# Kernel tuning notes

Hardware: AMD Instinct MI355X
Metric: run time of the kernel (lower is better)

## Reference

```python
import jax, jax.numpy as jnp
import numpy as np

B, T, L, F = 32, 512, 16, 128   # utterances, max frames, frame-spec width, specgram_height
H = 128                          # hidden_size1 == hidden_size2
C = 61                           # TIMIT phoneme count


def _p(key, shape, scale):
    return jax.random.normal(key, shape, jnp.float32) * scale


def setup_inputs() -> dict:
    key = jax.random.key(0)
    ks = jax.random.split(key, 32)
    s = 1.0 / np.sqrt(H)
    inp = {}
    inp["x"] = jax.random.normal(ks[0], (B, T, L, F), jnp.float32)
    inp["lengths"] = jax.random.randint(ks[1], (B,), T // 2, T + 1, jnp.int32)
    i = 2
    # rnn1: tanh-RNN, 2 layers, bidirectional (layer0 in=F, layer1 in=2H); dir axis 0
    for name, din in (("r1l0", F), ("r1l1", 2 * H)):
        inp[name + "_Wih"] = _p(ks[i], (2, H, din), s); i += 1
        inp[name + "_Whh"] = _p(ks[i], (2, H, H), s); i += 1
        inp[name + "_bih"] = _p(ks[i], (2, H), s); i += 1
        inp[name + "_bhh"] = _p(ks[i], (2, H), s); i += 1
    # rnn2: GRU, 2 layers, bidirectional (in=2H for both layers); gates packed r,z,n
    for name in ("g0", "g1"):
        inp[name + "_Wih"] = _p(ks[i], (2, 3 * H, 2 * H), s); i += 1
        inp[name + "_Whh"] = _p(ks[i], (2, 3 * H, H), s); i += 1
        inp[name + "_bih"] = _p(ks[i], (2, 3 * H), s); i += 1
        inp[name + "_bhh"] = _p(ks[i], (2, 3 * H), s); i += 1
    inp["fc_W"] = _p(ks[i], (C, 2 * H), s); i += 1
    inp["fc_b"] = _p(ks[i], (C,), s)
    return inp


def _rnn_bidir(x, Wih, Whh, bih, bhh):
    # x: (N, S, din) -> (N, S, 2H); PyTorch nn.RNN(tanh), bidirectional
    outs = []
    for d in range(2):
        xw = jnp.einsum('bli,hi->blh', x, Wih[d]) + bih[d]
        W, b = Whh[d], bhh[d]
        def step(h, xt):
            h = jnp.tanh(xt + h @ W.T + b)
            return h, h
        h0 = jnp.zeros((x.shape[0], W.shape[0]), x.dtype)
        _, ys = jax.lax.scan(step, h0, jnp.swapaxes(xw, 0, 1), reverse=(d == 1))
        outs.append(jnp.swapaxes(ys, 0, 1))
    return jnp.concatenate(outs, -1)


def _gru_bidir(x, Wih, Whh, bih, bhh):
    # x: (N, S, din) -> (N, S, 2H); PyTorch nn.GRU, bidirectional
    outs = []
    for d in range(2):
        xw = jnp.einsum('bli,hi->blh', x, Wih[d]) + bih[d]  # (N, S, 3H)
        W, b = Whh[d], bhh[d]
        def step(h, xt):
            g = h @ W.T + b
            xr, xz, xn = jnp.split(xt, 3, -1)
            gr, gz, gn = jnp.split(g, 3, -1)
            r = jax.nn.sigmoid(xr + gr)
            z = jax.nn.sigmoid(xz + gz)
            n = jnp.tanh(xn + r * gn)
            h = (1.0 - z) * n + z * h
            return h, h
        h0 = jnp.zeros((x.shape[0], W.shape[1]), x.dtype)
        _, ys = jax.lax.scan(step, h0, jnp.swapaxes(xw, 0, 1), reverse=(d == 1))
        outs.append(jnp.swapaxes(ys, 0, 1))
    return jnp.concatenate(outs, -1)


def reference(x, lengths,
              r1l0_Wih, r1l0_Whh, r1l0_bih, r1l0_bhh,
              r1l1_Wih, r1l1_Whh, r1l1_bih, r1l1_bhh,
              g0_Wih, g0_Whh, g0_bih, g0_bhh,
              g1_Wih, g1_Whh, g1_bih, g1_bhh,
              fc_W, fc_b):
    b, t, l, f = x.shape
    # per-sample rnn1 loop == one batched pass over all B*T frames (eval mode: no dropout)
    o = _rnn_bidir(x.reshape(b * t, l, f), r1l0_Wih, r1l0_Whh, r1l0_bih, r1l0_bhh)
    o = _rnn_bidir(o, r1l1_Wih, r1l1_Whh, r1l1_bih, r1l1_bhh)
    o = o[:, -1, :].reshape(b, t, 2 * H)       # last inner timestep per frame
    o = _gru_bidir(o, g0_Wih, g0_Whh, g0_bih, g0_bhh)
    o = _gru_bidir(o, g1_Wih, g1_Whh, g1_bih, g1_bhh)
    logits = o @ fc_W.T + fc_b                  # (B, T, C)
    mask = jnp.arange(t)[None, :] < lengths[:, None]
    # ragged scatter: concat first lengths[i] timesteps of each sample
    return logits.reshape(b * t, -1)[mask.reshape(-1)]
```

## Files before the change

kernel.cpp:

```cpp
#include <hip/hip_runtime.h>
#include <hip/hip_bf16.h>

#define B_ 32
#define T_ 512
#define L_ 16
#define F_ 128
#define H_ 128
#define C_ 61
#define NF_ (B_*T_)
#define CH_ 4096

typedef unsigned int u32;
typedef unsigned short u16;
typedef __attribute__((ext_vector_type(8))) short s16x8;
typedef __attribute__((ext_vector_type(4))) float f32x4;

__device__ __forceinline__ float bflo(u32 v){ return __uint_as_float(v << 16); }
__device__ __forceinline__ float bfhi(u32 v){ return __uint_as_float(v & 0xffff0000u); }
__device__ __forceinline__ u16 f2bf(float f){
  u32 u = __float_as_uint(f);
  u += 0x7fffu + ((u >> 16) & 1u);
  return (u16)(u >> 16);
}
__device__ __forceinline__ u32 pack2(float a, float b){
  return (u32)f2bf(a) | ((u32)f2bf(b) << 16);
}
__device__ __forceinline__ float fast_tanh(float x){
  float e = __expf(2.f*x);
  return 1.f - 2.f*__builtin_amdgcn_rcpf(e + 1.f);
}
__device__ __forceinline__ float fast_sigmoid(float x){
  return __builtin_amdgcn_rcpf(1.f + __expf(-x));
}
__device__ __forceinline__ f32x4 mfma16(s16x8 a, s16x8 b, f32x4 c){
  return __builtin_amdgcn_mfma_f32_16x16x32_bf16(a, b, c, 0, 0, 0);
}
__device__ __forceinline__ s16x8 packfrag(const float* p){
  const float4 a = *(const float4*)p;
  const float4 b = *(const float4*)(p+4);
  union { s16x8 v; u32 w[4]; } f;
  f.w[0]=pack2(a.x,a.y); f.w[1]=pack2(a.z,a.w);
  f.w[2]=pack2(b.x,b.y); f.w[3]=pack2(b.z,b.w);
  return f.v;
}

__global__ __launch_bounds__(256) void l0_mfma(
    const float* __restrict__ x,
    const float* __restrict__ Wih,
    const float* __restrict__ Whh,
    const float* __restrict__ bih,
    const float* __restrict__ bhh,
    u16* __restrict__ out)
{
  __shared__ __align__(16) u16 Hb[2][32][136];
  __shared__ __align__(16) u16 Xb[2][32][136];
  const int t = threadIdx.x;
  const int lane = t & 63, wv = t >> 6;
  const int l15 = lane & 15, kg = lane >> 4;
  const int dir = blockIdx.y;
  const int f0 = blockIdx.x * 32;
  s16x8 wih[2][4], whh[2][4];
  {
    const float* Wid = Wih + dir*16384;
    const float* Whd = Whh + dir*16384;
    #pragma unroll
    for (int nt = 0; nt < 2; nt++){
      const int u = wv*32 + nt*16 + l15;
      #pragma unroll
      for (int kc = 0; kc < 4; kc++){
        const int k = kc*32 + kg*8;
        wih[nt][kc] = packfrag(&Wid[u*128 + k]);
        whh[nt][kc] = packfrag(&Whd[u*128 + k]);
      }
    }
  }
  float bv[2];
  bv[0] = bih[dir*128 + wv*32 + l15]      + bhh[dir*128 + wv*32 + l15];
  bv[1] = bih[dir*128 + wv*32 + 16 + l15] + bhh[dir*128 + wv*32 + 16 + l15];
  const int sr = t >> 3, sc = (t & 7) * 16;
  {
    *(uint4*)&Hb[0][sr][sc]   = make_uint4(0,0,0,0);
    *(uint4*)&Hb[0][sr][sc+8] = make_uint4(0,0,0,0);
    const int s0 = dir ? 15 : 0;
    const float4* xp = (const float4*)&x[(size_t)(f0+sr)*2048 + s0*128 + sc];
    const float4 v0 = xp[0], v1 = xp[1], v2 = xp[2], v3 = xp[3];
    *(uint4*)&Xb[0][sr][sc]   = make_uint4(pack2(v0.x,v0.y),pack2(v0.z,v0.w),
                                           pack2(v1.x,v1.y),pack2(v1.z,v1.w));
    *(uint4*)&Xb[0][sr][sc+8] = make_uint4(pack2(v2.x,v2.y),pack2(v2.z,v2.w),
                                           pack2(v3.x,v3.y),pack2(v3.z,v3.w));
  }
  __syncthreads();
  int cur = 0;
  for (int st = 0; st < 16; st++){
    const int s = dir ? (15-st) : st;
    float4 p0,p1,p2,p3;
    if (st < 15){
      const int sn = dir ? (14-st) : (st+1);
      const float4* xp = (const float4*)&x[(size_t)(f0+sr)*2048 + sn*128 + sc];
      p0 = xp[0]; p1 = xp[1]; p2 = xp[2]; p3 = xp[3];
    }
    f32x4 acc00 = {0.f,0.f,0.f,0.f}, acc01 = acc00, acc10 = acc00, acc11 = acc00;
    #pragma unroll
    for (int kc = 0; kc < 4; kc++){
      const int ko = kc*32 + kg*8;
      const s16x8 ax0 = *(const s16x8*)&Xb[cur][l15][ko];
      const s16x8 ax1 = *(const s16x8*)&Xb[cur][16+l15][ko];
      const s16x8 ah0 = *(const s16x8*)&Hb[cur][l15][ko];
      const s16x8 ah1 = *(const s16x8*)&Hb[cur][16+l15][ko];
      acc00 = mfma16(ax0, wih[0][kc], acc00);
      acc01 = mfma16(ax0, wih[1][kc], acc01);
      acc10 = mfma16(ax1, wih[0][kc], acc10);
      acc11 = mfma16(ax1, wih[1][kc], acc11);
      acc00 = mfma16(ah0, whh[0][kc], acc00);
      acc01 = mfma16(ah0, whh[1][kc], acc01);
      acc10 = mfma16(ah1, whh[0][kc], acc10);
      acc11 = mfma16(ah1, whh[1][kc], acc11);
    }
    const int u0 = wv*32 + l15, u1 = wv*32 + 16 + l15;
    u16* op = out + (size_t)f0*4096 + s*256 + dir*128;
    #pragma unroll
    for (int r = 0; r < 4; r++){
      const int m0r = kg*4 + r, m1r = 16 + kg*4 + r;
      u16 h00 = f2bf(fast_tanh(acc00[r] + bv[0]));
      u16 h01 = f2bf(fast_tanh(acc01[r] + bv[1]));
      u16 h10 = f2bf(fast_tanh(acc10[r] + bv[0]));
      u16 h11 = f2bf(fast_tanh(acc11[r] + bv[1]));
      Hb[cur^1][m0r][u0] = h00;
      Hb[cur^1][m0r][u1] = h01;
      Hb[cur^1][m1r][u0] = h10;
      Hb[cur^1][m1r][u1] = h11;
      op[(size_t)m0r*4096 + u0] = h00;
      op[(size_t)m0r*4096 + u1] = h01;
      op[(size_t)m1r*4096 + u0] = h10;
      op[(size_t)m1r*4096 + u1] = h11;
    }
    if (st < 15){
      *(uint4*)&Xb[cur^1][sr][sc]   = make_uint4(pack2(p0.x,p0.y),pack2(p0.z,p0.w),
                                                 pack2(p1.x,p1.y),pack2(p1.z,p1.w));
      *(uint4*)&Xb[cur^1][sr][sc+8] = make_uint4(pack2(p2.x,p2.y),pack2(p2.z,p2.w),
                                                 pack2(p3.x,p3.y),pack2(p3.z,p3.w));
    }
    __syncthreads();
    cur ^= 1;
  }
}

__global__ __launch_bounds__(256) void l1f_mfma(
    const u16* __restrict__ U,
    const float* __restrict__ Wih,
    const float* __restrict__ Whh,
    const float* __restrict__ bih,
    const float* __restrict__ bhh,
    u16* __restrict__ out)
{
  __shared__ __align__(16) u16 Hb[2][16][136];
  __shared__ __align__(16) u16 Xb[2][16][264];
  const int t = threadIdx.x;
  const int lane = t & 63, wv = t >> 6;
  const int l15 = lane & 15, kg = lane >> 4;
  const int f0 = blockIdx.x * 16;
  s16x8 wih[2][8], whh[2][4];
  {
    #pragma unroll
    for (int nt = 0; nt < 2; nt++){
      const int u = wv*32 + nt*16 + l15;
      #pragma unroll
      for (int kc = 0; kc < 8; kc++)
        wih[nt][kc] = packfrag(&Wih[u*256 + kc*32 + kg*8]);
      #pragma unroll
      for (int kc = 0; kc < 4; kc++)
        whh[nt][kc] = packfrag(&Whh[u*128 + kc*32 + kg*8]);
    }
  }
  float bv[2];
  bv[0] = bih[wv*32 + l15]      + bhh[wv*32 + l15];
  bv[1] = bih[wv*32 + 16 + l15] + bhh[wv*32 + 16 + l15];
  const int sr = t >> 4, scu = (t & 15) * 16;
  for (int idx = t; idx < 272; idx += 256)
    ((uint4*)&Hb[0][0][0])[idx] = make_uint4(0,0,0,0);
  {
    const uint4* up = (const uint4*)&U[(size_t)(f0+sr)*4096 + scu];
    uint4 c0 = up[0], c1 = up[1];
    *(uint4*)&Xb[0][sr][scu]   = c0;
    *(uint4*)&Xb[0][sr][scu+8] = c1;
  }
  __syncthreads();
  int cur = 0;
  for (int st = 0; st < 16; st++){
    uint4 c0,c1;
    if (st < 15){
      const uint4* up = (const uint4*)&U[(size_t)(f0+sr)*4096 + (st+1)*256 + scu];
      c0 = up[0]; c1 = up[1];
    }
    f32x4 acc0 = {0.f,0.f,0.f,0.f}, acc1 = acc0;
    #pragma unroll
    for (int kc = 0; kc < 8; kc++){
      const s16x8 ax = *(const s16x8*)&Xb[cur][l15][kc*32 + kg*8];
      acc0 = mfma16(ax, wih[0][kc], acc0);
      acc1 = mfma16(ax, wih[1][kc], acc1);
    }
    #pragma unroll
    for (int kc = 0; kc < 4; kc++){
      const s16x8 ah = *(const s16x8*)&Hb[cur][l15][kc*32 + kg*8];
      acc0 = mfma16(ah, whh[0][kc], acc0);
      acc1 = mfma16(ah, whh[1][kc], acc1);
    }
    const int u0 = wv*32 + l15, u1 = wv*32 + 16 + l15;
    #pragma unroll
    for (int r = 0; r < 4; r++){
      const int m = kg*4 + r;
      const u16 h0 = f2bf(fast_tanh(acc0[r] + bv[0]));
      const u16 h1 = f2bf(fast_tanh(acc1[r] + bv[1]));
      Hb[cur^1][m][u0] = h0;
      Hb[cur^1][m][u1] = h1;
      if (st == 15){
        out[(size_t)(f0+m)*256 + u0] = h0;
        out[(size_t)(f0+m)*256 + u1] = h1;
      }
    }
    if (st < 15){
      *(uint4*)&Xb[cur^1][sr][scu]   = c0;
      *(uint4*)&Xb[cur^1][sr][scu+8] = c1;
    }
    __syncthreads();
    cur ^= 1;
  }
}

__global__ __launch_bounds__(256) void mfma_gemm(
    const u16* __restrict__ A, int lda,
    const u16* __restrict__ Wb, int K,
    const float* __restrict__ bias,
    float* __restrict__ Cf, u16* __restrict__ Cb, int ldc, int act)
{
  const int t = threadIdx.x;
  const int lane = t & 63, wv = t >> 6;
  const int l15 = lane & 15, kg = lane >> 4;
  const int n0 = blockIdx.x * 32;
  const int m0 = blockIdx.y * 64 + wv*16;
  const u16* Ap = A + (size_t)(m0 + l15)*lda + kg*8;
  const u16* W0 = Wb + (size_t)(n0 + l15)*K + kg*8;
  const u16* W1 = Wb + (size_t)(n0 + 16 + l15)*K + kg*8;
  f32x4 acc0 = {0.f,0.f,0.f,0.f}, acc1 = acc0;
  #pragma unroll 4
  for (int kc = 0; kc < K/32; kc++){
    const s16x8 a  = *(const s16x8*)(Ap + kc*32);
    const s16x8 b0 = *(const s16x8*)(W0 + kc*32);
    const s16x8 b1 = *(const s16x8*)(W1 + kc*32);
    acc0 = mfma16(a, b0, acc0);
    acc1 = mfma16(a, b1, acc1);
  }
  const int col0 = n0 + l15, col1 = n0 + 16 + l15;
  const float bv0 = bias[col0], bv1 = bias[col1];
  #pragma unroll
  for (int r = 0; r < 4; r++){
    const int row = m0 + kg*4 + r;
    float v0 = acc0[r] + bv0, v1 = acc1[r] + bv1;
    if (act){ v0 = fast_tanh(v0); v1 = fast_tanh(v1); }
    if (Cf){
      Cf[(size_t)row*ldc + col0] = v0;
      Cf[(size_t)row*ldc + col1] = v1;
    } else {
      Cb[(size_t)row*ldc + col0] = f2bf(v0);
      Cb[(size_t)row*ldc + col1] = f2bf(v1);
    }
  }
}

__global__ __launch_bounds__(256) void gemm_xw(
    const u16* __restrict__ A, int lda,
    const u16* __restrict__ Wb, int K,
    const float* __restrict__ bih, const float* __restrict__ bhhp,
    float* __restrict__ xwT)
{
  const int t = threadIdx.x;
  const int lane = t & 63, wv = t >> 6;
  const int l15 = lane & 15, kg = lane >> 4;
  const int n0 = blockIdx.x * 32;
  const int m0 = blockIdx.y * 64 + wv*16;
  const u16* Ap = A + (size_t)(m0 + l15)*lda + kg*8;
  const u16* W0 = Wb + (size_t)(n0 + l15)*K + kg*8;
  const u16* W1 = Wb + (size_t)(n0 + 16 + l15)*K + kg*8;
  f32x4 acc0 = {0.f,0.f,0.f,0.f}, acc1 = acc0;
  #pragma unroll 4
  for (int kc = 0; kc < K/32; kc++){
    const s16x8 a  = *(const s16x8*)(Ap + kc*32);
    const s16x8 b0 = *(const s16x8*)(W0 + kc*32);
    const s16x8 b1 = *(const s16x8*)(W1 + kc*32);
    acc0 = mfma16(a, b0, acc0);
    acc1 = mfma16(a, b1, acc1);
  }
  const int col0 = n0 + l15, col1 = n0 + 16 + l15;
  const int row0 = m0 + kg*4;
  const int b = row0 >> 9, tt0 = row0 & 511;
  const int half = b >> 4, bl = b & 15;
  float bv0 = bih[col0], bv1 = bih[col1];
  {
    const int c0 = col0 >= 384 ? col0-384 : col0;
    const int c1 = col1 >= 384 ? col1-384 : col1;
    if ((c0 >> 7) < 2) bv0 += bhhp[col0];
    if ((c1 >> 7) < 2) bv1 += bhhp[col1];
  }
  size_t i0, i1;
  {
    const int d0 = col0 >= 384 ? 1 : 0;
    const int c  = col0 - d0*384;
    const int g = c >> 7, cu = c & 127;
    i0 = (((((size_t)d0*512 + tt0)*2 + half)*4 + (cu>>5))*4 + ((cu>>2)&3))*384
         + (size_t)bl*24 + ((cu>>4)&1)*12 + g*4 + (cu&3);
  }
  {
    const int d1 = col1 >= 384 ? 1 : 0;
    const int c  = col1 - d1*384;
    const int g = c >> 7, cu = c & 127;
    i1 = (((((size_t)d1*512 + tt0)*2 + half)*4 + (cu>>5))*4 + ((cu>>2)&3))*384
         + (size_t)bl*24 + ((cu>>4)&1)*12 + g*4 + (cu&3);
  }
  #pragma unroll
  for (int r = 0; r < 4; r++){
    xwT[i0 + (size_t)r*12288] = acc0[r] + bv0;
    xwT[i1 + (size_t)r*12288] = acc1[r] + bv1;
  }
}

__global__ __launch_bounds__(256) void prep_kernel(
    const float* __restrict__ g0W, const float* __restrict__ g1W,
    const float* __restrict__ r1Wih,
    const float* __restrict__ r1bih, const float* __restrict__ r1bhh,
    u16* __restrict__ g0o, u16* __restrict__ g1o, u16* __restrict__ r1o,
    float* __restrict__ bo)
{
  const int i = blockIdx.x*256 + threadIdx.x;
  if (i < 196608){ g0o[i] = f2bf(g0W[i]); g1o[i] = f2bf(g1W[i]); }
  if (i < 32768)   r1o[i] = f2bf(r1Wih[32768 + i]);
  if (i < 128)     bo[i]  = r1bih[128+i] + r1bhh[128+i];
}

__global__ __launch_bounds__(256, 1) void gru_mfma(
    const float* __restrict__ xwT,
    const float* __restrict__ Whh,
    const float* __restrict__ bhh,
    u16* __restrict__ hout)
{
  __shared__ __align__(16) u16 h_lds[2][16][136];
  const int t = threadIdx.x;
  const int lane = t & 63, wv = t >> 6;
  const int l15 = lane & 15, kg = lane >> 4;
  const int dir = blockIdx.x & 1, half = blockIdx.x >> 1;
  s16x8 wa[2][3][4];
  {
    const float* Wd = Whh + (size_t)dir*49152;
    #pragma unroll
    for (int t2 = 0; t2 < 2; t2++)
      #pragma unroll
      for (int g = 0; g < 3; g++)
        #pragma unroll
        for (int kc = 0; kc < 4; kc++)
          wa[t2][g][kc] = packfrag(&Wd[(size_t)(g*128 + wv*32 + t2*16 + l15)*128
                                       + kc*32 + kg*8]);
  }
  f32x4 bhn[2];
  bhn[0] = *(const f32x4*)&bhh[dir*384 + 256 + wv*32 + kg*4];
  bhn[1] = *(const f32x4*)&bhh[dir*384 + 256 + wv*32 + 16 + kg*4];
  {
    const uint4 z = make_uint4(0,0,0,0);
    ((uint4*)h_lds)[t] = z;
    if (t < 16) ((uint4*)h_lds)[256 + t] = z;
  }
  f32x4 hreg[2] = {{0.f,0.f,0.f,0.f},{0.f,0.f,0.f,0.f}};
  const long tstep = dir ? -49152L : 49152L;
  const char* xb = (const char*)xwT
      + ((size_t)dir*512 + (dir ? 511 : 0))*49152
      + (size_t)((((half*4 + wv)*4 + kg)*16 + l15)*24)*4;
  f32x4 pa[6], pb[6];
  #pragma unroll
  for (int j = 0; j < 6; j++) pa[j] = *(const f32x4*)(xb + j*16);
  xb += tstep;
  #pragma unroll
  for (int j = 0; j < 6; j++) pb[j] = *(const f32x4*)(xb + j*16);
  xb += tstep;
  const int hstep = dir ? -256 : 256;
  int hoff = ((half*16 + l15)*512 + (dir ? 511 : 0))*256 + dir*128 + wv*32 + kg*4;
  __syncthreads();
  int cur = 0;

#define GSTEP(PX, DOLOAD)                                                   \
  {                                                                         \
    f32x4 acc[2][3] = {{{0.f,0.f,0.f,0.f},{0.f,0.f,0.f,0.f},               \
                        {0.f,0.f,0.f,0.f}},                                 \
                       {{0.f,0.f,0.f,0.f},{0.f,0.f,0.f,0.f},               \
                        {0.f,0.f,0.f,0.f}}};                                \
    _Pragma("unroll")                                                       \
    for (int kc = 0; kc < 4; kc++){                                         \
      const s16x8 hf = *(const s16x8*)&h_lds[cur][l15][kc*32 + kg*8];       \
      _Pragma("unroll")                                                     \
      for (int t2 = 0; t2 < 2; t2++)                                        \
        _Pragma("unroll")                                                   \
        for (int g = 0; g < 3; g++)                                         \
          acc[t2][g] = mfma16(wa[t2][g][kc], hf, acc[t2][g]);               \
    }                                                                       \
    f32x4 nx0,nx1,nx2,nx3,nx4,nx5;                                          \
    if (DOLOAD){                                                            \
      nx0 = *(const f32x4*)(xb);     nx1 = *(const f32x4*)(xb+16);          \
      nx2 = *(const f32x4*)(xb+32);  nx3 = *(const f32x4*)(xb+48);          \
      nx4 = *(const f32x4*)(xb+64);  nx5 = *(const f32x4*)(xb+80);          \
      xb += tstep;                                                          \
    }                                                                       \
    _Pragma("unroll")                                                       \
    for (int t2 = 0; t2 < 2; t2++){                                         \
      float hn[4];                                                          \
      _Pragma("unroll")                                                     \
      for (int r = 0; r < 4; r++){                                          \
        const float rr = fast_sigmoid(PX[t2*3+0][r] + acc[t2][0][r]);       \
        const float zz = fast_sigmoid(PX[t2*3+1][r] + acc[t2][1][r]);       \
        const float nn = fast_tanh(PX[t2*3+2][r]                            \
                                   + rr*(acc[t2][2][r] + bhn[t2][r]));      \
        hn[r] = fmaf(zz, hreg[t2][r] - nn, nn);                             \
        hreg[t2][r] = hn[r];                                                \
      }                                                                     \
      const uint2 hp = make_uint2(pack2(hn[0],hn[1]), pack2(hn[2],hn[3]));  \
      *(uint2*)&h_lds[cur^1][l15][wv*32 + t2*16 + kg*4] = hp;               \
      *(uint2*)&hout[hoff + t2*16] = hp;                                    \
    }                                                                       \
    hoff += hstep;                                                          \
    if (DOLOAD){                                                            \
      PX[0]=nx0; PX[1]=nx1; PX[2]=nx2; PX[3]=nx3; PX[4]=nx4; PX[5]=nx5;     \
    }                                                                       \
    __syncthreads();                                                        \
    cur ^= 1;                                                               \
  }

  for (int ti = 0; ti < 510; ti += 2){
    GSTEP(pa, 1);
    GSTEP(pb, 1);
  }
  GSTEP(pa, 0);
  GSTEP(pb, 0);
#undef GSTEP
}

__global__ void prefix_kernel(const int* __restrict__ lengths, int* __restrict__ pre){
  if (threadIdx.x == 0 && blockIdx.x == 0){
    int run = 0;
    for (int b = 0; b < 32; b++){ pre[b] = run; run += lengths[b]; }
  }
}

__global__ __launch_bounds__(256) void fc_kernel(
    const u16* __restrict__ A,
    const float* __restrict__ W,
    const float* __restrict__ bias,
    const int* __restrict__ lengths,
    const int* __restrict__ pre,
    float* __restrict__ out)
{
  __shared__ __align__(16) float4 Wl[64][61];
  __shared__ __align__(16) float  Al[64][256];
  const int t = threadIdx.x;
  const int row0 = blockIdx.x * 64;
  for (int idx = t; idx < 61*64; idx += 256){
    int c = idx >> 6, k4 = idx & 63;
    Wl[k4][c] = *(const float4*)&W[(size_t)c*256 + k4*4];
  }
  {
    const u32* A32 = (const u32*)(A + (size_t)row0*256);
    for (int idx = t; idx < 8192; idx += 256){
      u32 v = A32[idx];
      int r = idx >> 7, kp = idx & 127;
      Al[r][2*kp]   = bflo(v);
      Al[r][2*kp+1] = bfhi(v);
    }
  }
  __syncthreads();
  const int c = t & 63;
  const int rbase = t >> 6;
  if (c < 61){
    const float bv = bias[c];
    for (int rr = rbase; rr < 64; rr += 4){
      float s0=0,s1=0,s2=0,s3=0;
      const float4* Ap = (const float4*)&Al[rr][0];
      #pragma unroll
      for (int k4 = 0; k4 < 64; k4++){
        const float4 w = Wl[k4][c];
        const float4 a = Ap[k4];
        s0 = fmaf(w.x, a.x, s0);
        s1 = fmaf(w.y, a.y, s1);
        s2 = fmaf(w.z, a.z, s2);
        s3 = fmaf(w.w, a.w, s3);
      }
      const int n = row0 + rr;
      const int b = n >> 9, tt = n & 511;
      if (tt < lengths[b])
        out[(size_t)(pre[b] + tt)*61 + c] = bv + s0+s1+s2+s3;
    }
  }
}

extern "C" void kernel_launch(void* const* d_in, const int* in_sizes, int n_in,
                              void* d_out, int out_size, void* d_ws, size_t ws_size,
                              hipStream_t stream)
{
  const float* x     = (const float*)d_in[0];
  const int*   lens  = (const int*)d_in[1];
  const float* r0Wih = (const float*)d_in[2];
  const float* r0Whh = (const float*)d_in[3];
  const float* r0bih = (const float*)d_in[4];
  const float* r0bhh = (const float*)d_in[5];
  const float* r1Wih = (const float*)d_in[6];
  const float* r1Whh = (const float*)d_in[7];
  const float* r1bih = (const float*)d_in[8];
  const float* r1bhh = (const float*)d_in[9];
  const float* g0Wih = (const float*)d_in[10];
  const float* g0Whh = (const float*)d_in[11];
  const float* g0bih = (const float*)d_in[12];
  const float* g0bhh = (const float*)d_in[13];
  const float* g1Wih = (const float*)d_in[14];
  const float* g1Whh = (const float*)d_in[15];
  const float* g1bih = (const float*)d_in[16];
  const float* g1bhh = (const float*)d_in[17];
  const float* fcW   = (const float*)d_in[18];
  const float* fcb   = (const float*)d_in[19];
  float* out = (float*)d_out;

  char* ws = (char*)d_ws;
  u16*   l0buf = (u16*)(ws);
  float* xwbuf = (float*)(ws);
  u16*   g0out = (u16*)(ws + 50331648);
  u16*   g0Wb  = (u16*)(ws + 58720256);
  u16*   g1Wb  = (u16*)(ws + 58720256 + 393216);
  u16*   r1Wb  = (u16*)(ws + 58720256 + 786432);
  float* biasb = (float*)(ws + 58720256 + 851968);
  u16*   g1out = (u16*)(ws + 58720256);
  u16*   rnn1  = (u16*)(ws + 67108864);
  int*   pre   = (int*)(ws + 75497472);

  prep_kernel<<<768, 256, 0, stream>>>(g0Wih, g1Wih, r1Wih, r1bih, r1bhh,
                                       g0Wb, g1Wb, r1Wb, biasb);
  for (int c = 0; c < NF_/CH_; c++){
    l0_mfma<<<dim3(CH_/32, 2), 256, 0, stream>>>(
        x + (size_t)c*CH_*2048, r0Wih, r0Whh, r0bih, r0bhh, l0buf);
    l1f_mfma<<<dim3(CH_/16), 256, 0, stream>>>(
        l0buf, r1Wih, r1Whh, r1bih, r1bhh, rnn1 + (size_t)c*CH_*256);
    mfma_gemm<<<dim3(128/32, CH_/64), 256, 0, stream>>>(
        l0buf + 15*256, 4096, r1Wb, 256, biasb,
        (float*)nullptr, rnn1 + (size_t)c*CH_*256 + 128, 256, 1);
  }
  gemm_xw<<<dim3(768/32, NF_/64), 256, 0, stream>>>(
      rnn1, 256, g0Wb, 256, g0bih, g0bhh, xwbuf);
  gru_mfma<<<4, 256, 0, stream>>>(xwbuf, g0Whh, g0bhh, g0out);
  gemm_xw<<<dim3(768/32, NF_/64), 256, 0, stream>>>(
      g0out, 256, g1Wb, 256, g1bih, g1bhh, xwbuf);
  gru_mfma<<<4, 256, 0, stream>>>(xwbuf, g1Whh, g1bhh, g1out);
  prefix_kernel<<<1, 64, 0, stream>>>(lens, pre);
  fc_kernel<<<NF_/64, 256, 0, stream>>>(g1out, fcW, fcb, lens, pre, out);
}
```

Baseline: 1.191 ms.

## Split GRU recurrence across 8 waves, halve l0 tile, use lgkm-only barriers

The latency-bound GRU recurrence now launches 512 threads per block, so each wave owns 16 hidden units instead of 32. This halves the serial MFMA chain and gate math per timestep, and the xw layout written by gemm_xw is rearranged to match. The layer-0 RNN kernel processes 16 frames per block instead of 32, doubling the block count to raise parallelism. __syncthreads is replaced by a barrier that waits only on LDS counters, avoiding stalls on outstanding global loads. The trade-off is more barrier participants per step in the GRU and relying on correct waitcnt semantics for the prefetched global loads.

```diff
diff --git a/kernel.cpp b/kernel.cpp
--- a/kernel.cpp
+++ b/kernel.cpp
@@ -35,6 +35,9 @@
 __device__ __forceinline__ f32x4 mfma16(s16x8 a, s16x8 b, f32x4 c){
   return __builtin_amdgcn_mfma_f32_16x16x32_bf16(a, b, c, 0, 0, 0);
 }
+__device__ __forceinline__ void lds_barrier(){
+  asm volatile("s_waitcnt lgkmcnt(0)\n\ts_barrier" ::: "memory");
+}
 __device__ __forceinline__ s16x8 packfrag(const float* p){
   const float4 a = *(const float4*)p;
   const float4 b = *(const float4*)(p+4);
@@ -52,13 +55,13 @@
     const float* __restrict__ bhh,
     u16* __restrict__ out)
 {
-  __shared__ __align__(16) u16 Hb[2][32][136];
-  __shared__ __align__(16) u16 Xb[2][32][136];
+  __shared__ __align__(16) u16 Hb[2][16][136];
+  __shared__ __align__(16) u16 Xb[2][16][136];
   const int t = threadIdx.x;
   const int lane = t & 63, wv = t >> 6;
   const int l15 = lane & 15, kg = lane >> 4;
   const int dir = blockIdx.y;
-  const int f0 = blockIdx.x * 32;
+  const int f0 = blockIdx.x * 16;
   s16x8 wih[2][4], whh[2][4];
   {
     const float* Wid = Wih + dir*16384;
@@ -77,70 +80,54 @@
   float bv[2];
   bv[0] = bih[dir*128 + wv*32 + l15]      + bhh[dir*128 + wv*32 + l15];
   bv[1] = bih[dir*128 + wv*32 + 16 + l15] + bhh[dir*128 + wv*32 + 16 + l15];
-  const int sr = t >> 3, sc = (t & 7) * 16;
-  {
-    *(uint4*)&Hb[0][sr][sc]   = make_uint4(0,0,0,0);
-    *(uint4*)&Hb[0][sr][sc+8] = make_uint4(0,0,0,0);
+  const int sr = t >> 4, sc8 = (t & 15) * 8;
+  for (int idx = t; idx < 272; idx += 256)
+    ((uint4*)&Hb[0][0][0])[idx] = make_uint4(0,0,0,0);
+  {
     const int s0 = dir ? 15 : 0;
-    const float4* xp = (const float4*)&x[(size_t)(f0+sr)*2048 + s0*128 + sc];
-    const float4 v0 = xp[0], v1 = xp[1], v2 = xp[2], v3 = xp[3];
-    *(uint4*)&Xb[0][sr][sc]   = make_uint4(pack2(v0.x,v0.y),pack2(v0.z,v0.w),
-                                           pack2(v1.x,v1.y),pack2(v1.z,v1.w));
-    *(uint4*)&Xb[0][sr][sc+8] = make_uint4(pack2(v2.x,v2.y),pack2(v2.z,v2.w),
-                                           pack2(v3.x,v3.y),pack2(v3.z,v3.w));
-  }
-  __syncthreads();
+    const float4* xp = (const float4*)&x[(size_t)(f0+sr)*2048 + s0*128 + sc8];
+    const float4 v0 = xp[0], v1 = xp[1];
+    *(uint4*)&Xb[0][sr][sc8] = make_uint4(pack2(v0.x,v0.y),pack2(v0.z,v0.w),
+                                          pack2(v1.x,v1.y),pack2(v1.z,v1.w));
+  }
+  lds_barrier();
   int cur = 0;
   for (int st = 0; st < 16; st++){
     const int s = dir ? (15-st) : st;
-    float4 p0,p1,p2,p3;
+    float4 p0,p1;
     if (st < 15){
       const int sn = dir ? (14-st) : (st+1);
-      const float4* xp = (const float4*)&x[(size_t)(f0+sr)*2048 + sn*128 + sc];
-      p0 = xp[0]; p1 = xp[1]; p2 = xp[2]; p3 = xp[3];
-    }
-    f32x4 acc00 = {0.f,0.f,0.f,0.f}, acc01 = acc00, acc10 = acc00, acc11 = acc00;
+      const float4* xp = (const float4*)&x[(size_t)(f0+sr)*2048 + sn*128 + sc8];
+      p0 = xp[0]; p1 = xp[1];
+    }
+    f32x4 acc0 = {0.f,0.f,0.f,0.f}, acc1 = acc0;
     #pragma unroll
     for (int kc = 0; kc < 4; kc++){
       const int ko = kc*32 + kg*8;
-      const s16x8 ax0 = *(const s16x8*)&Xb[cur][l15][ko];
-      const s16x8 ax1 = *(const s16x8*)&Xb[cur][16+l15][ko];
-      const s16x8 ah0 = *(const s16x8*)&Hb[cur][l15][ko];
-      const s16x8 ah1 = *(const s16x8*)&Hb[cur][16+l15][ko];
-      acc00 = mfma16(ax0, wih[0][kc], acc00);
-      acc01 = mfma16(ax0, wih[1][kc], acc01);
-      acc10 = mfma16(ax1, wih[0][kc], acc10);
-      acc11 = mfma16(ax1, wih[1][kc], acc11);
-      acc00 = mfma16(ah0, whh[0][kc], acc00);
-      acc01 = mfma16(ah0, whh[1][kc], acc01);
-      acc10 = mfma16(ah1, whh[0][kc], acc10);
-      acc11 = mfma16(ah1, whh[1][kc], acc11);
+      const s16x8 ax = *(const s16x8*)&Xb[cur][l15][ko];
+      const s16x8 ah = *(const s16x8*)&Hb[cur][l15][ko];
+      acc0 = mfma16(ax, wih[0][kc], acc0);
+      acc1 = mfma16(ax, wih[1][kc], acc1);
+      acc0 = mfma16(ah, whh[0][kc], acc0);
+      acc1 = mfma16(ah, whh[1][kc], acc1);
     }
     const int u0 = wv*32 + l15, u1 = wv*32 + 16 + l15;
     u16* op = out + (size_t)f0*4096 + s*256 + dir*128;
     #pragma unroll
     for (int r = 0; r < 4; r++){
-      const int m0r = kg*4 + r, m1r = 16 + kg*4 + r;
-      u16 h00 = f2bf(fast_tanh(acc00[r] + bv[0]));
-      u16 h01 = f2bf(fast_tanh(acc01[r] + bv[1]));
-      u16 h10 = f2bf(fast_tanh(acc10[r] + bv[0]));
-      u16 h11 = f2bf(fast_tanh(acc11[r] + bv[1]));
-      Hb[cur^1][m0r][u0] = h00;
-      Hb[cur^1][m0r][u1] = h01;
-      Hb[cur^1][m1r][u0] = h10;
-      Hb[cur^1][m1r][u1] = h11;
-      op[(size_t)m0r*4096 + u0] = h00;
-      op[(size_t)m0r*4096 + u1] = h01;
-      op[(size_t)m1r*4096 + u0] = h10;
-      op[(size_t)m1r*4096 + u1] = h11;
+      const int m = kg*4 + r;
+      const u16 h0 = f2bf(fast_tanh(acc0[r] + bv[0]));
+      const u16 h1 = f2bf(fast_tanh(acc1[r] + bv[1]));
+      Hb[cur^1][m][u0] = h0;
+      Hb[cur^1][m][u1] = h1;
+      op[(size_t)m*4096 + u0] = h0;
+      op[(size_t)m*4096 + u1] = h1;
     }
     if (st < 15){
-      *(uint4*)&Xb[cur^1][sr][sc]   = make_uint4(pack2(p0.x,p0.y),pack2(p0.z,p0.w),
-                                                 pack2(p1.x,p1.y),pack2(p1.z,p1.w));
-      *(uint4*)&Xb[cur^1][sr][sc+8] = make_uint4(pack2(p2.x,p2.y),pack2(p2.z,p2.w),
-                                                 pack2(p3.x,p3.y),pack2(p3.z,p3.w));
-    }
-    __syncthreads();
+      *(uint4*)&Xb[cur^1][sr][sc8] = make_uint4(pack2(p0.x,p0.y),pack2(p0.z,p0.w),
+                                                pack2(p1.x,p1.y),pack2(p1.z,p1.w));
+    }
+    lds_barrier();
     cur ^= 1;
   }
 }
@@ -184,7 +171,7 @@
     *(uint4*)&Xb[0][sr][scu]   = c0;
     *(uint4*)&Xb[0][sr][scu+8] = c1;
   }
-  __syncthreads();
+  lds_barrier();
   int cur = 0;
   for (int st = 0; st < 16; st++){
     uint4 c0,c1;
@@ -222,7 +209,7 @@
       *(uint4*)&Xb[cur^1][sr][scu]   = c0;
       *(uint4*)&Xb[cur^1][sr][scu+8] = c1;
     }
-    __syncthreads();
+    lds_barrier();
     cur ^= 1;
   }
 }
@@ -306,15 +293,15 @@
     const int d0 = col0 >= 384 ? 1 : 0;
     const int c  = col0 - d0*384;
     const int g = c >> 7, cu = c & 127;
-    i0 = (((((size_t)d0*512 + tt0)*2 + half)*4 + (cu>>5))*4 + ((cu>>2)&3))*384
-         + (size_t)bl*24 + ((cu>>4)&1)*12 + g*4 + (cu&3);
+    i0 = (((size_t)d0*512 + tt0)*2 + half)*6144
+         + (size_t)(((cu>>4)*4 + ((cu>>2)&3))*16 + bl)*12 + g*4 + (cu&3);
   }
   {
     const int d1 = col1 >= 384 ? 1 : 0;
     const int c  = col1 - d1*384;
     const int g = c >> 7, cu = c & 127;
-    i1 = (((((size_t)d1*512 + tt0)*2 + half)*4 + (cu>>5))*4 + ((cu>>2)&3))*384
-         + (size_t)bl*24 + ((cu>>4)&1)*12 + g*4 + (cu&3);
+    i1 = (((size_t)d1*512 + tt0)*2 + half)*6144
+         + (size_t)(((cu>>4)*4 + ((cu>>2)&3))*16 + bl)*12 + g*4 + (cu&3);
   }
   #pragma unroll
   for (int r = 0; r < 4; r++){
@@ -336,7 +323,7 @@
   if (i < 128)     bo[i]  = r1bih[128+i] + r1bhh[128+i];
 }
 
-__global__ __launch_bounds__(256, 1) void gru_mfma(
+__global__ __launch_bounds__(512, 1) void gru_mfma(
     const float* __restrict__ xwT,
     const float* __restrict__ Whh,
     const float* __restrict__ bhh,
@@ -347,86 +334,65 @@
   const int lane = t & 63, wv = t >> 6;
   const int l15 = lane & 15, kg = lane >> 4;
   const int dir = blockIdx.x & 1, half = blockIdx.x >> 1;
-  s16x8 wa[2][3][4];
+  s16x8 wa[3][4];
   {
     const float* Wd = Whh + (size_t)dir*49152;
     #pragma unroll
-    for (int t2 = 0; t2 < 2; t2++)
+    for (int g = 0; g < 3; g++)
       #pragma unroll
-      for (int g = 0; g < 3; g++)
-        #pragma unroll
-        for (int kc = 0; kc < 4; kc++)
-          wa[t2][g][kc] = packfrag(&Wd[(size_t)(g*128 + wv*32 + t2*16 + l15)*128
-                                       + kc*32 + kg*8]);
-  }
-  f32x4 bhn[2];
-  bhn[0] = *(const f32x4*)&bhh[dir*384 + 256 + wv*32 + kg*4];
-  bhn[1] = *(const f32x4*)&bhh[dir*384 + 256 + wv*32 + 16 + kg*4];
-  {
-    const uint4 z = make_uint4(0,0,0,0);
-    ((uint4*)h_lds)[t] = z;
-    if (t < 16) ((uint4*)h_lds)[256 + t] = z;
-  }
-  f32x4 hreg[2] = {{0.f,0.f,0.f,0.f},{0.f,0.f,0.f,0.f}};
+      for (int kc = 0; kc < 4; kc++)
+        wa[g][kc] = packfrag(&Wd[(size_t)(g*128 + wv*16 + l15)*128
+                                 + kc*32 + kg*8]);
+  }
+  const f32x4 bhn = *(const f32x4*)&bhh[dir*384 + 256 + wv*16 + kg*4];
+  if (t < 272) ((uint4*)h_lds)[t] = make_uint4(0,0,0,0);
+  f32x4 hreg = {0.f,0.f,0.f,0.f};
   const long tstep = dir ? -49152L : 49152L;
   const char* xb = (const char*)xwT
-      + ((size_t)dir*512 + (dir ? 511 : 0))*49152
-      + (size_t)((((half*4 + wv)*4 + kg)*16 + l15)*24)*4;
-  f32x4 pa[6], pb[6];
-  #pragma unroll
-  for (int j = 0; j < 6; j++) pa[j] = *(const f32x4*)(xb + j*16);
+      + (((size_t)dir*512 + (dir ? 511 : 0))*2 + half)*24576
+      + (size_t)(((wv*4 + kg)*16 + l15)*12)*4;
+  f32x4 pa[3], pb[3];
+  pa[0] = *(const f32x4*)(xb); pa[1] = *(const f32x4*)(xb+16); pa[2] = *(const f32x4*)(xb+32);
   xb += tstep;
-  #pragma unroll
-  for (int j = 0; j < 6; j++) pb[j] = *(const f32x4*)(xb + j*16);
+  pb[0] = *(const f32x4*)(xb); pb[1] = *(const f32x4*)(xb+16); pb[2] = *(const f32x4*)(xb+32);
   xb += tstep;
   const int hstep = dir ? -256 : 256;
-  int hoff = ((half*16 + l15)*512 + (dir ? 511 : 0))*256 + dir*128 + wv*32 + kg*4;
-  __syncthreads();
+  int hoff = ((half*16 + l15)*512 + (dir ? 511 : 0))*256 + dir*128 + wv*16 + kg*4;
+  lds_barrier();
   int cur = 0;
 
 #define GSTEP(PX, DOLOAD)                                                   \
   {                                                                         \
-    f32x4 acc[2][3] = {{{0.f,0.f,0.f,0.f},{0.f,0.f,0.f,0.f},               \
-                        {0.f,0.f,0.f,0.f}},                                 \
-                       {{0.f,0.f,0.f,0.f},{0.f,0.f,0.f,0.f},               \
-                        {0.f,0.f,0.f,0.f}}};                                \
+        \
+    const f32x4 cxr = PX[0], cxz = PX[1], cxn = PX[2];                      \
+    if (DOLOAD){                                                            \
+      PX[0] = *(const f32x4*)(xb);                                          \
+      PX[1] = *(const f32x4*)(xb+16);                                       \
+      PX[2] = *(const f32x4*)(xb+32);                                       \
+      xb += tstep;                                                          \
+    }                                                                       \
+    f32x4 a0 = {0.f,0.f,0.f,0.f}, a1 = a0, a2 = a0;                         \
     _Pragma("unroll")                                                       \
     for (int kc = 0; kc < 4; kc++){                                         \
       const s16x8 hf = *(const s16x8*)&h_lds[cur][l15][kc*32 + kg*8];       \
-      _Pragma("unroll")                                                     \
-      for (int t2 = 0; t2 < 2; t2++)                                        \
-        _Pragma("unroll")                                                   \
-        for (int g = 0; g < 3; g++)                                         \
-          acc[t2][g] = mfma16(wa[t2][g][kc], hf, acc[t2][g]);               \
+      a0 = mfma16(wa[0][kc], hf, a0);                                       \
+      a1 = mfma16(wa[1][kc], hf, a1);                                       \
+      a2 = mfma16(wa[2][kc], hf, a2);                                       \
     }                                                                       \
-    f32x4 nx0,nx1,nx2,nx3,nx4,nx5;                                          \
-    if (DOLOAD){                                                            \
-      nx0 = *(const f32x4*)(xb);     nx1 = *(const f32x4*)(xb+16);          \
-      nx2 = *(const f32x4*)(xb+32);  nx3 = *(const f32x4*)(xb+48);          \
-      nx4 = *(const f32x4*)(xb+64);  nx5 = *(const f32x4*)(xb+80);          \
-      xb += tstep;                                                          \
+    float hn[4];                                                            \
+    _Pragma("unroll")                                                       \
+    for (int r = 0; r < 4; r++){                                            \
+      const float rr = fast_sigmoid(cxr[r] + a0[r]);                        \
+      const float zz = fast_sigmoid(cxz[r] + a1[r]);                        \
+      const float nn = fast_tanh(cxn[r] + rr*(a2[r] + bhn[r]));             \
+      hn[r] = fmaf(zz, hreg[r] - nn, nn);                                   \
+      hreg[r] = hn[r];                                                      \
     }                                                                       \
-    _Pragma("unroll")                                                       \
-    for (int t2 = 0; t2 < 2; t2++){                                         \
-      float hn[4];                                                          \
-      _Pragma("unroll")                                                     \
-      for (int r = 0; r < 4; r++){                                          \
-        const float rr = fast_sigmoid(PX[t2*3+0][r] + acc[t2][0][r]);       \
-        const float zz = fast_sigmoid(PX[t2*3+1][r] + acc[t2][1][r]);       \
-        const float nn = fast_tanh(PX[t2*3+2][r]                            \
-                                   + rr*(acc[t2][2][r] + bhn[t2][r]));      \
-        hn[r] = fmaf(zz, hreg[t2][r] - nn, nn);                             \
-        hreg[t2][r] = hn[r];                                                \
-      }                                                                     \
-      const uint2 hp = make_uint2(pack2(hn[0],hn[1]), pack2(hn[2],hn[3]));  \
-      *(uint2*)&h_lds[cur^1][l15][wv*32 + t2*16 + kg*4] = hp;               \
-      *(uint2*)&hout[hoff + t2*16] = hp;                                    \
-    }                                                                       \
+    const uint2 hp = make_uint2(pack2(hn[0],hn[1]), pack2(hn[2],hn[3]));    \
+    *(uint2*)&h_lds[cur^1][l15][wv*16 + kg*4] = hp;                         \
+    *(uint2*)&hout[hoff] = hp;                                              \
     hoff += hstep;                                                          \
-    if (DOLOAD){                                                            \
-      PX[0]=nx0; PX[1]=nx1; PX[2]=nx2; PX[3]=nx3; PX[4]=nx4; PX[5]=nx5;     \
-    }                                                                       \
-    __syncthreads();                                                        \
+    lds_barrier();                                                          \
     cur ^= 1;                                                               \
   }
 
@@ -537,7 +503,7 @@
   prep_kernel<<<768, 256, 0, stream>>>(g0Wih, g1Wih, r1Wih, r1bih, r1bhh,
                                        g0Wb, g1Wb, r1Wb, biasb);
   for (int c = 0; c < NF_/CH_; c++){
-    l0_mfma<<<dim3(CH_/32, 2), 256, 0, stream>>>(
+    l0_mfma<<<dim3(CH_/16, 2), 256, 0, stream>>>(
         x + (size_t)c*CH_*2048, r0Wih, r0Whh, r0bih, r0bhh, l0buf);
     l1f_mfma<<<dim3(CH_/16), 256, 0, stream>>>(
         l0buf, r1Wih, r1Whh, r1bih, r1bhh, rnn1 + (size_t)c*CH_*256);
@@ -547,10 +513,10 @@
   }
   gemm_xw<<<dim3(768/32, NF_/64), 256, 0, stream>>>(
       rnn1, 256, g0Wb, 256, g0bih, g0bhh, xwbuf);
-  gru_mfma<<<4, 256, 0, stream>>>(xwbuf, g0Whh, g0bhh, g0out);
+  gru_mfma<<<4, 512, 0, stream>>>(xwbuf, g0Whh, g0bhh, g0out);
   gemm_xw<<<dim3(768/32, NF_/64), 256, 0, stream>>>(
       g0out, 256, g1Wb, 256, g1bih, g1bhh, xwbuf);
-  gru_mfma<<<4, 256, 0, stream>>>(xwbuf, g1Whh, g1bhh, g1out);
+  gru_mfma<<<4, 512, 0, stream>>>(xwbuf, g1Whh, g1bhh, g1out);
   prefix_kernel<<<1, 64, 0, stream>>>(lens, pre);
   fc_kernel<<<NF_/64, 256, 0, stream>>>(g1out, fcW, fcb, lens, pre, out);
 }
```

Result: faster. 1.033 ms (-13.2%).
